# Kernel optimization log

Hardware: AMD Instinct MI355X
Metric: run time of the kernel (lower is better)

Reference implementation:

```python
import jax, jax.numpy as jnp
import numpy as np

N_SRC = [700000, 51200, 5120]
N_DST = [51200, 5120, 1024]
N_EDGE = [768000, 51200, 5120]
IN_FEATS, N_HIDDEN, N_CLASSES = 128, 256, 47


def setup_inputs() -> dict:
    key = jax.random.key(0)
    ks = jax.random.split(key, 16)
    inp = {}
    inp["x"] = jax.random.normal(ks[0], (N_SRC[0], IN_FEATS), dtype=jnp.float32)
    # edge lists per block: src indexes block-src nodes, dst indexes block-dst nodes
    for l in range(3):
        inp[f"src{l}"] = jax.random.randint(ks[1 + 2 * l], (N_EDGE[l],), 0, N_SRC[l], dtype=jnp.int32)
        inp[f"dst{l}"] = jax.random.randint(ks[2 + 2 * l], (N_EDGE[l],), 0, N_DST[l], dtype=jnp.int32)
    dims = [(IN_FEATS, N_HIDDEN), (N_HIDDEN, N_HIDDEN), (N_HIDDEN, N_CLASSES)]
    for l, (di, do) in enumerate(dims):
        scale = 1.0 / np.sqrt(di)
        inp[f"Ws{l}"] = jax.random.normal(ks[7 + 3 * l], (di, do), dtype=jnp.float32) * scale
        inp[f"Wn{l}"] = jax.random.normal(ks[8 + 3 * l], (di, do), dtype=jnp.float32) * scale
        inp[f"b{l}"] = jnp.zeros((do,), dtype=jnp.float32)
    return inp


def _sage_conv(h, src, dst, n_dst, Ws, Wn, b):
    # mean-aggregate neighbor (src) features onto dst nodes, then dual linear
    h_dst = h[:n_dst]                                   # dst nodes are a prefix of src nodes
    msg = jax.ops.segment_sum(h[src], dst, num_segments=n_dst)
    deg = jax.ops.segment_sum(jnp.ones((src.shape[0], 1), h.dtype), dst, num_segments=n_dst)
    h_neigh = msg / jnp.maximum(deg, 1.0)               # zero-degree dst -> 0 (DGL convention)
    return h_dst @ Ws + h_neigh @ Wn + b


def reference(x, src0, dst0, src1, dst1, src2, dst2,
              Ws0, Wn0, b0, Ws1, Wn1, b1, Ws2, Wn2, b2):
    h = _sage_conv(x, src0, dst0, N_DST[0], Ws0, Wn0, b0)
    h = jax.nn.relu(h)  # dropout = identity in eval
    h = _sage_conv(h, src1, dst1, N_DST[1], Ws1, Wn1, b1)
    h = jax.nn.relu(h)
    h = _sage_conv(h, src2, dst2, N_DST[2], Ws2, Wn2, b2)
    return h
```

## Files before the change

kernel.cpp:

```cpp
#include <hip/hip_runtime.h>


typedef __bf16 bf16x8 __attribute__((ext_vector_type(8)));
typedef float f32x4 __attribute__((ext_vector_type(4)));

static __device__ __forceinline__ unsigned short f32_to_bf16(float f) {
    unsigned u = __float_as_uint(f);
    u += 0x7fffu + ((u >> 16) & 1u);
    return (unsigned short)(u >> 16);
}
static __device__ __forceinline__ float bf16lo(unsigned u) { return __uint_as_float(u << 16); }
static __device__ __forceinline__ float bf16hi(unsigned u) { return __uint_as_float(u & 0xffff0000u); }

__global__ void sage_prep(const float* __restrict__ Ws0, const float* __restrict__ Wn0,
                          const float* __restrict__ Ws1, const float* __restrict__ Wn1,
                          const float* __restrict__ Ws2, const float* __restrict__ Wn2,
                          unsigned short* __restrict__ WT0, unsigned short* __restrict__ WT1,
                          unsigned short* __restrict__ WT2,
                          const int* __restrict__ d0, int* __restrict__ c0,
                          const int* __restrict__ d1, int* __restrict__ c1,
                          const int* __restrict__ d2, int* __restrict__ c2) {
    const int b = blockIdx.x;
    if (b < 256) {
        int idx = b * 256 + threadIdx.x;
        int n = idx >> 8, k = idx & 255;
        float v = (k < 128) ? Ws0[(size_t)k * 256 + n] : Wn0[(size_t)(k - 128) * 256 + n];
        WT0[idx] = f32_to_bf16(v);
    } else if (b < 768) {
        int idx = (b - 256) * 256 + threadIdx.x;
        int n = idx >> 9, k = idx & 511;
        float v = (k < 256) ? Ws1[(size_t)k * 256 + n] : Wn1[(size_t)(k - 256) * 256 + n];
        WT1[idx] = f32_to_bf16(v);
    } else if (b < 862) {
        int idx = (b - 768) * 256 + threadIdx.x;
        int n = idx >> 9, k = idx & 511;
        float v = (k < 256) ? Ws2[(size_t)k * 47 + n] : Wn2[(size_t)(k - 256) * 47 + n];
        WT2[idx] = f32_to_bf16(v);
    } else if (b < 2362) {
        int i = (b - 862) * 256 + threadIdx.x;
        int2 d = ((const int2*)d0)[i];
        atomicAdd(&c0[d.x], 1);
        atomicAdd(&c0[d.y], 1);
    } else if (b < 2462) {
        int i = (b - 2362) * 256 + threadIdx.x;
        int2 d = ((const int2*)d1)[i];
        atomicAdd(&c1[d.x], 1);
        atomicAdd(&c1[d.y], 1);
    } else {
        int i = (b - 2462) * 256 + threadIdx.x;
        int2 d = ((const int2*)d2)[i];
        atomicAdd(&c2[d.x], 1);
        atomicAdd(&c2[d.y], 1);
    }
}

__launch_bounds__(1024)
__global__ void sage_scanfill(const int* __restrict__ c0, int* __restrict__ o0, int* __restrict__ u0,
                              const int* __restrict__ c1, int* __restrict__ o1, int* __restrict__ u1,
                              const int* __restrict__ c2, int* __restrict__ o2, int* __restrict__ u2,
                              int* __restrict__ sync,
                              const int* __restrict__ s0, const int* __restrict__ d0, int* __restrict__ r0,
                              const int* __restrict__ s1, const int* __restrict__ d1, int* __restrict__ r1,
                              const int* __restrict__ s2, const int* __restrict__ d2, int* __restrict__ r2) {
    const int b = blockIdx.x;
    const int tid = threadIdx.x;
    const int lane = tid & 63;
    const int wid = tid >> 6;
    const int* counts; int* off; int* cur; int chunk, first, nblk, n;
    if (b < 50)      { counts = c0; off = o0; cur = u0; chunk = b;      first = 0;  nblk = 50; n = 51200; }
    else if (b < 55) { counts = c1; off = o1; cur = u1; chunk = b - 50; first = 50; nblk = 5;  n = 5120;  }
    else             { counts = c2; off = o2; cur = u2; chunk = 0;      first = 55; nblk = 1;  n = 1024;  }

    const int idx = chunk * 1024 + tid;
    const int v = counts[idx];

    int incl = v;
#pragma unroll
    for (int d = 1; d < 64; d <<= 1) {
        int t = __shfl_up(incl, d, 64);
        if (lane >= d) incl += t;
    }

    __shared__ int wsum[16];
    __shared__ int s_base;
    if (lane == 63) wsum[wid] = incl;
    __syncthreads();

    if (tid < 64) {
        int s = (lane < 16) ? wsum[lane] : 0;
        int inc = s;
#pragma unroll
        for (int d = 1; d < 16; d <<= 1) {
            int t = __shfl_up(inc, d, 64);
            if (lane >= d) inc += t;
        }
        if (lane < 16) wsum[lane] = inc - s;
        if (lane == 15) {
            __hip_atomic_store(&sync[16 + b], inc, __ATOMIC_RELEASE, __HIP_MEMORY_SCOPE_AGENT);
            __hip_atomic_fetch_add(&sync[0], 1, __ATOMIC_RELEASE, __HIP_MEMORY_SCOPE_AGENT);
        }
    }
    if (tid == 0) {
        while (__hip_atomic_load(&sync[0], __ATOMIC_ACQUIRE, __HIP_MEMORY_SCOPE_AGENT) < 56)
            __builtin_amdgcn_s_sleep(2);
    }
    __syncthreads();

    if (tid < 64) {
        int p = (lane < chunk)
            ? __hip_atomic_load(&sync[16 + first + lane], __ATOMIC_RELAXED, __HIP_MEMORY_SCOPE_AGENT)
            : 0;
#pragma unroll
        for (int d = 32; d >= 1; d >>= 1) p += __shfl_down(p, d, 64);
        if (lane == 0) s_base = p;
    }
    __syncthreads();

    const int excl = s_base + wsum[wid] + (incl - v);
    off[idx] = excl;
    __hip_atomic_store(&cur[idx], excl, __ATOMIC_RELAXED, __HIP_MEMORY_SCOPE_AGENT);
    if (chunk == nblk - 1 && tid == 1023) off[n] = excl + v;

    __syncthreads();
    if (tid == 0) {
        __hip_atomic_fetch_add(&sync[1], 1, __ATOMIC_RELEASE, __HIP_MEMORY_SCOPE_AGENT);
        while (__hip_atomic_load(&sync[1], __ATOMIC_ACQUIRE, __HIP_MEMORY_SCOPE_AGENT) < 56)
            __builtin_amdgcn_s_sleep(2);
    }
    __syncthreads();

    const int gtid = b * 1024 + tid;
    for (int i = gtid; i < 412160; i += 57344) {
        const int* sp; const int* dp; int* up; int* rp; int ii;
        if (i < 384000)      { sp = s0; dp = d0; up = u0; rp = r0; ii = i; }
        else if (i < 409600) { sp = s1; dp = d1; up = u1; rp = r1; ii = i - 384000; }
        else                 { sp = s2; dp = d2; up = u2; rp = r2; ii = i - 409600; }
        int2 s = ((const int2*)sp)[ii];
        int2 d = ((const int2*)dp)[ii];
        int p0 = atomicAdd(&up[d.x], 1);
        int p1 = atomicAdd(&up[d.y], 1);
        rp[p0] = s.x;
        rp[p1] = s.y;
    }
}

__global__ void sage_gather0(const float* __restrict__ x, const int* __restrict__ csr,
                             const int* __restrict__ off, unsigned short* __restrict__ out,
                             int n_dst) {
    int row = (blockIdx.x * 256 + threadIdx.x) >> 6;
    if (row >= n_dst) return;
    const int lane = threadIdx.x & 63;
    const int half = lane >> 5;
    const int fl = lane & 31;
    const int beg = off[row], end = off[row + 1];
    const float4* hp = (const float4*)x + fl;
    float4 accA = make_float4(0.f, 0.f, 0.f, 0.f);
    float4 accB = make_float4(0.f, 0.f, 0.f, 0.f);
    int i = beg;
    for (; i + 7 < end; i += 8) {
        int s0 = csr[i + half];
        int s1 = csr[i + 2 + half];
        int s2 = csr[i + 4 + half];
        int s3 = csr[i + 6 + half];
        float4 v0 = hp[(size_t)s0 * 32];
        float4 v1 = hp[(size_t)s1 * 32];
        float4 v2 = hp[(size_t)s2 * 32];
        float4 v3 = hp[(size_t)s3 * 32];
        accA.x += v0.x; accA.y += v0.y; accA.z += v0.z; accA.w += v0.w;
        accB.x += v1.x; accB.y += v1.y; accB.z += v1.z; accB.w += v1.w;
        accA.x += v2.x; accA.y += v2.y; accA.z += v2.z; accA.w += v2.w;
        accB.x += v3.x; accB.y += v3.y; accB.z += v3.z; accB.w += v3.w;
    }
    for (; i + 1 < end; i += 2) {
        int s = csr[i + half];
        float4 v = hp[(size_t)s * 32];
        accA.x += v.x; accA.y += v.y; accA.z += v.z; accA.w += v.w;
    }
    if (i < end && half == 0) {
        int s = csr[i];
        float4 v = hp[(size_t)s * 32];
        accA.x += v.x; accA.y += v.y; accA.z += v.z; accA.w += v.w;
    }
    accA.x += accB.x; accA.y += accB.y; accA.z += accB.z; accA.w += accB.w;
    accA.x += __shfl_down(accA.x, 32);
    accA.y += __shfl_down(accA.y, 32);
    accA.z += __shfl_down(accA.z, 32);
    accA.w += __shfl_down(accA.w, 32);
    if (half == 0) {
        float inv = 1.0f / fmaxf((float)(end - beg), 1.0f);
        uint2 o;
        o.x = (unsigned)f32_to_bf16(accA.x * inv) | ((unsigned)f32_to_bf16(accA.y * inv) << 16);
        o.y = (unsigned)f32_to_bf16(accA.z * inv) | ((unsigned)f32_to_bf16(accA.w * inv) << 16);
        ((uint2*)out)[(size_t)row * 32 + fl] = o;
    }
}

__global__ void sage_gather256(const unsigned short* __restrict__ h, const int* __restrict__ csr,
                               const int* __restrict__ off, unsigned short* __restrict__ out,
                               int n_dst) {
    int row = (blockIdx.x * 256 + threadIdx.x) >> 6;
    if (row >= n_dst) return;
    const int lane = threadIdx.x & 63;
    const int half = lane >> 5;
    const int fl = lane & 31;
    const int beg = off[row], end = off[row + 1];
    const uint4* hp = (const uint4*)h + fl;
    float a[8] = {0.f, 0.f, 0.f, 0.f, 0.f, 0.f, 0.f, 0.f};
    float b[8] = {0.f, 0.f, 0.f, 0.f, 0.f, 0.f, 0.f, 0.f};
    int i = beg;
    for (; i + 3 < end; i += 4) {
        int s0 = csr[i + half];
        int s1 = csr[i + 2 + half];
        uint4 u0 = hp[(size_t)s0 * 32];
        uint4 u1 = hp[(size_t)s1 * 32];
        a[0] += bf16lo(u0.x); a[1] += bf16hi(u0.x);
        a[2] += bf16lo(u0.y); a[3] += bf16hi(u0.y);
        a[4] += bf16lo(u0.z); a[5] += bf16hi(u0.z);
        a[6] += bf16lo(u0.w); a[7] += bf16hi(u0.w);
        b[0] += bf16lo(u1.x); b[1] += bf16hi(u1.x);
        b[2] += bf16lo(u1.y); b[3] += bf16hi(u1.y);
        b[4] += bf16lo(u1.z); b[5] += bf16hi(u1.z);
        b[6] += bf16lo(u1.w); b[7] += bf16hi(u1.w);
    }
    for (; i + 1 < end; i += 2) {
        int s = csr[i + half];
        uint4 u = hp[(size_t)s * 32];
        a[0] += bf16lo(u.x); a[1] += bf16hi(u.x);
        a[2] += bf16lo(u.y); a[3] += bf16hi(u.y);
        a[4] += bf16lo(u.z); a[5] += bf16hi(u.z);
        a[6] += bf16lo(u.w); a[7] += bf16hi(u.w);
    }
    if (i < end && half == 0) {
        int s = csr[i];
        uint4 u = hp[(size_t)s * 32];
        a[0] += bf16lo(u.x); a[1] += bf16hi(u.x);
        a[2] += bf16lo(u.y); a[3] += bf16hi(u.y);
        a[4] += bf16lo(u.z); a[5] += bf16hi(u.z);
        a[6] += bf16lo(u.w); a[7] += bf16hi(u.w);
    }
#pragma unroll
    for (int k = 0; k < 8; ++k) { a[k] += b[k]; a[k] += __shfl_down(a[k], 32); }
    if (half == 0) {
        float inv = 1.0f / fmaxf((float)(end - beg), 1.0f);
        uint4 o;
        o.x = (unsigned)f32_to_bf16(a[0] * inv) | ((unsigned)f32_to_bf16(a[1] * inv) << 16);
        o.y = (unsigned)f32_to_bf16(a[2] * inv) | ((unsigned)f32_to_bf16(a[3] * inv) << 16);
        o.z = (unsigned)f32_to_bf16(a[4] * inv) | ((unsigned)f32_to_bf16(a[5] * inv) << 16);
        o.w = (unsigned)f32_to_bf16(a[6] * inv) | ((unsigned)f32_to_bf16(a[7] * inv) << 16);
        ((uint4*)out)[(size_t)row * 32 + fl] = o;
    }
}

template <int RELU, int OUT_BF16, int A_FP32>
__launch_bounds__(256)
__global__ void sage_gemm(const unsigned short* __restrict__ Hdst,
                          const float* __restrict__ Hdst32,
                          const unsigned short* __restrict__ Hneigh,
                          const unsigned short* __restrict__ WT,
                          const float* __restrict__ bias,
                          void* __restrict__ Out,
                          int N, int K1) {
    const int Ktot = 2 * K1;
    __shared__ unsigned short smem[2][128][72];
    unsigned short (*As)[72] = smem[0];
    unsigned short (*Bs)[72] = smem[1];

    const int t = threadIdx.x;
    const int lane = t & 63;
    const int w = t >> 6;
    const int wm = (w >> 1) * 64;
    const int wn = (w & 1) * 64;
    const int bm = blockIdx.y * 128;
    const int bn = blockIdx.x * 128;

    const int rowL = t >> 1;
    const int kL = (t & 1) * 32;

    f32x4 acc[4][4] = {};

    const int ktiles = Ktot >> 6;
    for (int kt = 0; kt < ktiles; ++kt) {
        const int k0 = kt << 6;
        if (A_FP32 && k0 < K1) {
            const float* src = Hdst32 + (size_t)(bm + rowL) * K1 + k0 + kL;
#pragma unroll
            for (int q = 0; q < 4; ++q) {
                float4 fa = ((const float4*)src)[q * 2];
                float4 fb = ((const float4*)src)[q * 2 + 1];
                uint4 o;
                o.x = (unsigned)f32_to_bf16(fa.x) | ((unsigned)f32_to_bf16(fa.y) << 16);
                o.y = (unsigned)f32_to_bf16(fa.z) | ((unsigned)f32_to_bf16(fa.w) << 16);
                o.z = (unsigned)f32_to_bf16(fb.x) | ((unsigned)f32_to_bf16(fb.y) << 16);
                o.w = (unsigned)f32_to_bf16(fb.z) | ((unsigned)f32_to_bf16(fb.w) << 16);
                *(uint4*)&As[rowL][kL + q * 8] = o;
            }
        } else {
            const unsigned short* src = (k0 < K1)
                ? (Hdst + (size_t)(bm + rowL) * K1 + k0 + kL)
                : (Hneigh + (size_t)(bm + rowL) * K1 + (k0 - K1) + kL);
            uint4 v0 = *(const uint4*)src;
            uint4 v1 = *(const uint4*)(src + 8);
            uint4 v2 = *(const uint4*)(src + 16);
            uint4 v3 = *(const uint4*)(src + 24);
            *(uint4*)&As[rowL][kL]      = v0;
            *(uint4*)&As[rowL][kL + 8]  = v1;
            *(uint4*)&As[rowL][kL + 16] = v2;
            *(uint4*)&As[rowL][kL + 24] = v3;
        }
        {
            int n = bn + rowL;
            uint4 v0 = {0,0,0,0}, v1 = {0,0,0,0}, v2 = {0,0,0,0}, v3 = {0,0,0,0};
            if (n < N) {
                const unsigned short* srcB = WT + (size_t)n * Ktot + k0 + kL;
                v0 = *(const uint4*)srcB;
                v1 = *(const uint4*)(srcB + 8);
                v2 = *(const uint4*)(srcB + 16);
                v3 = *(const uint4*)(srcB + 24);
            }
            *(uint4*)&Bs[rowL][kL]      = v0;
            *(uint4*)&Bs[rowL][kL + 8]  = v1;
            *(uint4*)&Bs[rowL][kL + 16] = v2;
            *(uint4*)&Bs[rowL][kL + 24] = v3;
        }
        __syncthreads();

        const int fr = lane & 15;
        const int fk = (lane >> 4) * 8;
#pragma unroll
        for (int ks = 0; ks < 64; ks += 32) {
            bf16x8 av[4], bv[4];
#pragma unroll
            for (int mt = 0; mt < 4; ++mt) av[mt] = *(const bf16x8*)&As[wm + mt * 16 + fr][ks + fk];
#pragma unroll
            for (int nt = 0; nt < 4; ++nt) bv[nt] = *(const bf16x8*)&Bs[wn + nt * 16 + fr][ks + fk];
#pragma unroll
            for (int mt = 0; mt < 4; ++mt)
#pragma unroll
                for (int nt = 0; nt < 4; ++nt)
                    acc[mt][nt] = __builtin_amdgcn_mfma_f32_16x16x32_bf16(av[mt], bv[nt], acc[mt][nt], 0, 0, 0);
        }
        __syncthreads();
    }

    const int quad = lane >> 4;
    const int colL = lane & 15;
    if (OUT_BF16 && N == 256) {
        unsigned short* C = (unsigned short*)smem;
#pragma unroll
        for (int mt = 0; mt < 4; ++mt)
#pragma unroll
            for (int nt = 0; nt < 4; ++nt)
#pragma unroll
                for (int r = 0; r < 4; ++r) {
                    int lrow = wm + mt * 16 + quad * 4 + r;
                    int lcol = wn + nt * 16 + colL;
                    float v = acc[mt][nt][r] + bias[bn + lcol];
                    if (RELU) v = fmaxf(v, 0.0f);
                    C[lrow * 136 + lcol] = f32_to_bf16(v);
                }
        __syncthreads();
        unsigned short* o = (unsigned short*)Out;
#pragma unroll
        for (int c = 0; c < 8; ++c) {
            int chunk = t * 8 + c;
            int row = chunk >> 4, cc = chunk & 15;
            uint4 v = *(const uint4*)&C[row * 136 + cc * 8];
            *(uint4*)(o + (size_t)(bm + row) * N + bn + cc * 8) = v;
        }
    } else {
#pragma unroll
        for (int mt = 0; mt < 4; ++mt)
#pragma unroll
            for (int nt = 0; nt < 4; ++nt)
#pragma unroll
                for (int r = 0; r < 4; ++r) {
                    int grow = bm + wm + mt * 16 + quad * 4 + r;
                    int gcol = bn + wn + nt * 16 + colL;
                    if (gcol < N) {
                        float v = acc[mt][nt][r] + bias[gcol];
                        if (RELU) v = fmaxf(v, 0.0f);
                        if (OUT_BF16) ((unsigned short*)Out)[(size_t)grow * N + gcol] = f32_to_bf16(v);
                        else ((float*)Out)[(size_t)grow * N + gcol] = v;
                    }
                }
    }
}


extern "C" void kernel_launch(void* const* d_in, const int* in_sizes, int n_in,
                              void* d_out, int out_size, void* d_ws, size_t ws_size,
                              hipStream_t stream) {
    const float* x    = (const float*)d_in[0];
    const int* src0 = (const int*)d_in[1];
    const int* dst0 = (const int*)d_in[2];
    const int* src1 = (const int*)d_in[3];
    const int* dst1 = (const int*)d_in[4];
    const int* src2 = (const int*)d_in[5];
    const int* dst2 = (const int*)d_in[6];
    const float* Ws0 = (const float*)d_in[7];
    const float* Wn0 = (const float*)d_in[8];
    const float* b0  = (const float*)d_in[9];
    const float* Ws1 = (const float*)d_in[10];
    const float* Wn1 = (const float*)d_in[11];
    const float* b1  = (const float*)d_in[12];
    const float* Ws2 = (const float*)d_in[13];
    const float* Wn2 = (const float*)d_in[14];
    const float* b2  = (const float*)d_in[15];
    float* out = (float*)d_out;

    char* ws = (char*)d_ws;
    unsigned short* h1      = (unsigned short*)(ws + 13107200);
    unsigned short* h2      = (unsigned short*)(ws + 39321600);
    unsigned short* hneigh0 = (unsigned short*)(ws + 41943040);
    unsigned short* hneigh1 = (unsigned short*)(ws + 55050240);
    unsigned short* hneigh2 = (unsigned short*)(ws + 57671680);
    unsigned short* WT0     = (unsigned short*)(ws + 58195968);
    unsigned short* WT1     = (unsigned short*)(ws + 58327040);
    unsigned short* WT2     = (unsigned short*)(ws + 58589184);
    int* counts0 = (int*)(ws + 58637312);
    int* counts1 = (int*)(ws + 58842112);
    int* counts2 = (int*)(ws + 58862592);
    int* syncp   = (int*)(ws + 58866688);
    int* off0    = (int*)(ws + 58870784);
    int* off1    = (int*)(ws + 59075600);
    int* off2    = (int*)(ws + 59096096);
    int* cur0    = (int*)(ws + 59100208);
    int* cur1    = (int*)(ws + 59305008);
    int* cur2    = (int*)(ws + 59325488);
    int* csr0    = (int*)(ws + 59329584);
    int* csr1    = (int*)(ws + 62401584);
    int* csr2    = (int*)(ws + 62606384);

    hipMemsetAsync(counts0, 0, 233472, stream);

    sage_prep<<<2472, 256, 0, stream>>>(Ws0, Wn0, Ws1, Wn1, Ws2, Wn2,
                                        WT0, WT1, WT2,
                                        dst0, counts0, dst1, counts1, dst2, counts2);
    sage_scanfill<<<56, 1024, 0, stream>>>(counts0, off0, cur0, counts1, off1, cur1,
                                           counts2, off2, cur2, syncp,
                                           src0, dst0, csr0,
                                           src1, dst1, csr1,
                                           src2, dst2, csr2);

    sage_gather0<<<12800, 256, 0, stream>>>(x, csr0, off0, hneigh0, 51200);
    { dim3 g(2, 400); sage_gemm<1, 1, 1><<<g, 256, 0, stream>>>(nullptr, x, hneigh0, WT0, b0, h1, 256, 128); }

    sage_gather256<<<1280, 256, 0, stream>>>(h1, csr1, off1, hneigh1, 5120);
    { dim3 g(2, 40); sage_gemm<1, 1, 0><<<g, 256, 0, stream>>>(h1, nullptr, hneigh1, WT1, b1, h2, 256, 256); }

    sage_gather256<<<256, 256, 0, stream>>>(h2, csr2, off2, hneigh2, 1024);
    { dim3 g(1, 8); sage_gemm<0, 0, 0><<<g, 256, 0, stream>>>(h2, nullptr, hneigh2, WT2, b2, out, 47, 256); }
}
```

Measured before the change: 669.0 us.

## Fuse weight prep, degree count, scan and CSR fill into one grid-synced kernel

Merges the separate prep and scan/fill kernels into one persistent 256×1024 kernel that uses global atomic barriers between phases. The CSR fill now runs across all 256 blocks instead of 56. The same kernel also pre-casts the first 51200 rows of x to bf16, so the layer-0 GEMM reads bf16 instead of converting fp32 inline. This removes a launch and widens the atomic-bound fill phase. In exchange it adds an extra pass over x, more grid-wide spin barriers, and relies on all 256 large blocks being resident at once.

```diff
diff --git a/kernel.cpp b/kernel.cpp
--- a/kernel.cpp
+++ b/kernel.cpp
@@ -12,125 +12,143 @@
 static __device__ __forceinline__ float bf16lo(unsigned u) { return __uint_as_float(u << 16); }
 static __device__ __forceinline__ float bf16hi(unsigned u) { return __uint_as_float(u & 0xffff0000u); }
 
-__global__ void sage_prep(const float* __restrict__ Ws0, const float* __restrict__ Wn0,
-                          const float* __restrict__ Ws1, const float* __restrict__ Wn1,
-                          const float* __restrict__ Ws2, const float* __restrict__ Wn2,
-                          unsigned short* __restrict__ WT0, unsigned short* __restrict__ WT1,
-                          unsigned short* __restrict__ WT2,
-                          const int* __restrict__ d0, int* __restrict__ c0,
-                          const int* __restrict__ d1, int* __restrict__ c1,
-                          const int* __restrict__ d2, int* __restrict__ c2) {
-    const int b = blockIdx.x;
-    if (b < 256) {
-        int idx = b * 256 + threadIdx.x;
-        int n = idx >> 8, k = idx & 255;
-        float v = (k < 128) ? Ws0[(size_t)k * 256 + n] : Wn0[(size_t)(k - 128) * 256 + n];
-        WT0[idx] = f32_to_bf16(v);
-    } else if (b < 768) {
-        int idx = (b - 256) * 256 + threadIdx.x;
-        int n = idx >> 9, k = idx & 511;
-        float v = (k < 256) ? Ws1[(size_t)k * 256 + n] : Wn1[(size_t)(k - 256) * 256 + n];
-        WT1[idx] = f32_to_bf16(v);
-    } else if (b < 862) {
-        int idx = (b - 768) * 256 + threadIdx.x;
-        int n = idx >> 9, k = idx & 511;
-        float v = (k < 256) ? Ws2[(size_t)k * 47 + n] : Wn2[(size_t)(k - 256) * 47 + n];
-        WT2[idx] = f32_to_bf16(v);
-    } else if (b < 2362) {
-        int i = (b - 862) * 256 + threadIdx.x;
-        int2 d = ((const int2*)d0)[i];
-        atomicAdd(&c0[d.x], 1);
-        atomicAdd(&c0[d.y], 1);
-    } else if (b < 2462) {
-        int i = (b - 2362) * 256 + threadIdx.x;
-        int2 d = ((const int2*)d1)[i];
-        atomicAdd(&c1[d.x], 1);
-        atomicAdd(&c1[d.y], 1);
-    } else {
-        int i = (b - 2462) * 256 + threadIdx.x;
-        int2 d = ((const int2*)d2)[i];
-        atomicAdd(&c2[d.x], 1);
-        atomicAdd(&c2[d.y], 1);
-    }
-}
-
 __launch_bounds__(1024)
-__global__ void sage_scanfill(const int* __restrict__ c0, int* __restrict__ o0, int* __restrict__ u0,
-                              const int* __restrict__ c1, int* __restrict__ o1, int* __restrict__ u1,
-                              const int* __restrict__ c2, int* __restrict__ o2, int* __restrict__ u2,
-                              int* __restrict__ sync,
-                              const int* __restrict__ s0, const int* __restrict__ d0, int* __restrict__ r0,
-                              const int* __restrict__ s1, const int* __restrict__ d1, int* __restrict__ r1,
-                              const int* __restrict__ s2, const int* __restrict__ d2, int* __restrict__ r2) {
+__global__ void sage_csr(const float* __restrict__ x, unsigned short* __restrict__ xcast,
+                         const float* __restrict__ Ws0, const float* __restrict__ Wn0,
+                         const float* __restrict__ Ws1, const float* __restrict__ Wn1,
+                         const float* __restrict__ Ws2, const float* __restrict__ Wn2,
+                         unsigned short* __restrict__ WT0, unsigned short* __restrict__ WT1,
+                         unsigned short* __restrict__ WT2,
+                         const int* __restrict__ s0, const int* __restrict__ d0,
+                         const int* __restrict__ s1, const int* __restrict__ d1,
+                         const int* __restrict__ s2, const int* __restrict__ d2,
+                         int* __restrict__ c0, int* __restrict__ o0, int* __restrict__ u0,
+                         int* __restrict__ c1, int* __restrict__ o1, int* __restrict__ u1,
+                         int* __restrict__ c2, int* __restrict__ o2, int* __restrict__ u2,
+                         int* __restrict__ r0, int* __restrict__ r1, int* __restrict__ r2,
+                         int* __restrict__ sync) {
     const int b = blockIdx.x;
     const int tid = threadIdx.x;
-    const int lane = tid & 63;
-    const int wid = tid >> 6;
-    const int* counts; int* off; int* cur; int chunk, first, nblk, n;
-    if (b < 50)      { counts = c0; off = o0; cur = u0; chunk = b;      first = 0;  nblk = 50; n = 51200; }
-    else if (b < 55) { counts = c1; off = o1; cur = u1; chunk = b - 50; first = 50; nblk = 5;  n = 5120;  }
-    else             { counts = c2; off = o2; cur = u2; chunk = 0;      first = 55; nblk = 1;  n = 1024;  }
-
-    const int idx = chunk * 1024 + tid;
-    const int v = counts[idx];
-
-    int incl = v;
-#pragma unroll
-    for (int d = 1; d < 64; d <<= 1) {
-        int t = __shfl_up(incl, d, 64);
-        if (lane >= d) incl += t;
-    }
-
-    __shared__ int wsum[16];
-    __shared__ int s_base;
-    if (lane == 63) wsum[wid] = incl;
-    __syncthreads();
-
-    if (tid < 64) {
-        int s = (lane < 16) ? wsum[lane] : 0;
-        int inc = s;
-#pragma unroll
-        for (int d = 1; d < 16; d <<= 1) {
-            int t = __shfl_up(inc, d, 64);
-            if (lane >= d) inc += t;
-        }
-        if (lane < 16) wsum[lane] = inc - s;
-        if (lane == 15) {
-            __hip_atomic_store(&sync[16 + b], inc, __ATOMIC_RELEASE, __HIP_MEMORY_SCOPE_AGENT);
-            __hip_atomic_fetch_add(&sync[0], 1, __ATOMIC_RELEASE, __HIP_MEMORY_SCOPE_AGENT);
-        }
-    }
-    if (tid == 0) {
-        while (__hip_atomic_load(&sync[0], __ATOMIC_ACQUIRE, __HIP_MEMORY_SCOPE_AGENT) < 56)
-            __builtin_amdgcn_s_sleep(2);
-    }
-    __syncthreads();
-
-    if (tid < 64) {
-        int p = (lane < chunk)
-            ? __hip_atomic_load(&sync[16 + first + lane], __ATOMIC_RELAXED, __HIP_MEMORY_SCOPE_AGENT)
-            : 0;
-#pragma unroll
-        for (int d = 32; d >= 1; d >>= 1) p += __shfl_down(p, d, 64);
-        if (lane == 0) s_base = p;
-    }
-    __syncthreads();
-
-    const int excl = s_base + wsum[wid] + (incl - v);
-    off[idx] = excl;
-    __hip_atomic_store(&cur[idx], excl, __ATOMIC_RELAXED, __HIP_MEMORY_SCOPE_AGENT);
-    if (chunk == nblk - 1 && tid == 1023) off[n] = excl + v;
+    const int gtid = b * 1024 + tid;
+
+    for (int u = gtid; u < 2271232; u += 262144) {
+        if (u < 1638400) {
+            float4 v = ((const float4*)x)[u];
+            uint2 o;
+            o.x = (unsigned)f32_to_bf16(v.x) | ((unsigned)f32_to_bf16(v.y) << 16);
+            o.y = (unsigned)f32_to_bf16(v.z) | ((unsigned)f32_to_bf16(v.w) << 16);
+            ((uint2*)xcast)[u] = o;
+        } else if (u < 1859072) {
+            int i = u - 1638400;
+            if (i < 65536) {
+                int n = i >> 8, k = i & 255;
+                float v = (k < 128) ? Ws0[(size_t)k * 256 + n] : Wn0[(size_t)(k - 128) * 256 + n];
+                WT0[i] = f32_to_bf16(v);
+            } else if (i < 196608) {
+                int j = i - 65536;
+                int n = j >> 9, k = j & 511;
+                float v = (k < 256) ? Ws1[(size_t)k * 256 + n] : Wn1[(size_t)(k - 256) * 256 + n];
+                WT1[j] = f32_to_bf16(v);
+            } else {
+                int j = i - 196608;
+                int n = j >> 9, k = j & 511;
+                float v = (k < 256) ? Ws2[(size_t)k * 47 + n] : Wn2[(size_t)(k - 256) * 47 + n];
+                WT2[j] = f32_to_bf16(v);
+            }
+        } else {
+            int p = u - 1859072;
+            if (p < 384000) {
+                int2 d = ((const int2*)d0)[p];
+                atomicAdd(&c0[d.x], 1);
+                atomicAdd(&c0[d.y], 1);
+            } else if (p < 409600) {
+                int2 d = ((const int2*)d1)[p - 384000];
+                atomicAdd(&c1[d.x], 1);
+                atomicAdd(&c1[d.y], 1);
+            } else {
+                int2 d = ((const int2*)d2)[p - 409600];
+                atomicAdd(&c2[d.x], 1);
+                atomicAdd(&c2[d.y], 1);
+            }
+        }
+    }
 
     __syncthreads();
     if (tid == 0) {
-        __hip_atomic_fetch_add(&sync[1], 1, __ATOMIC_RELEASE, __HIP_MEMORY_SCOPE_AGENT);
-        while (__hip_atomic_load(&sync[1], __ATOMIC_ACQUIRE, __HIP_MEMORY_SCOPE_AGENT) < 56)
+        __hip_atomic_fetch_add(&sync[0], 1, __ATOMIC_RELEASE, __HIP_MEMORY_SCOPE_AGENT);
+        while (__hip_atomic_load(&sync[0], __ATOMIC_ACQUIRE, __HIP_MEMORY_SCOPE_AGENT) < 256)
             __builtin_amdgcn_s_sleep(2);
     }
     __syncthreads();
 
-    const int gtid = b * 1024 + tid;
-    for (int i = gtid; i < 412160; i += 57344) {
+    if (b < 56) {
+        const int lane = tid & 63;
+        const int wid = tid >> 6;
+        const int* counts; int* off; int* cur; int chunk, first, nblk, n;
+        if (b < 50)      { counts = c0; off = o0; cur = u0; chunk = b;      first = 0;  nblk = 50; n = 51200; }
+        else if (b < 55) { counts = c1; off = o1; cur = u1; chunk = b - 50; first = 50; nblk = 5;  n = 5120;  }
+        else             { counts = c2; off = o2; cur = u2; chunk = 0;      first = 55; nblk = 1;  n = 1024;  }
+
+        const int idx = chunk * 1024 + tid;
+        const int v = __hip_atomic_load(&counts[idx], __ATOMIC_RELAXED, __HIP_MEMORY_SCOPE_AGENT);
+
+        int incl = v;
+#pragma unroll
+        for (int d = 1; d < 64; d <<= 1) {
+            int t = __shfl_up(incl, d, 64);
+            if (lane >= d) incl += t;
+        }
+
+        __shared__ int wsum[16];
+        __shared__ int s_base;
+        if (lane == 63) wsum[wid] = incl;
+        __syncthreads();
+
+        if (tid < 64) {
+            int s = (lane < 16) ? wsum[lane] : 0;
+            int inc = s;
+#pragma unroll
+            for (int d = 1; d < 16; d <<= 1) {
+                int t = __shfl_up(inc, d, 64);
+                if (lane >= d) inc += t;
+            }
+            if (lane < 16) wsum[lane] = inc - s;
+            if (lane == 15) {
+                __hip_atomic_store(&sync[16 + b], inc, __ATOMIC_RELEASE, __HIP_MEMORY_SCOPE_AGENT);
+                __hip_atomic_fetch_add(&sync[1], 1, __ATOMIC_RELEASE, __HIP_MEMORY_SCOPE_AGENT);
+            }
+        }
+        if (tid == 0) {
+            while (__hip_atomic_load(&sync[1], __ATOMIC_ACQUIRE, __HIP_MEMORY_SCOPE_AGENT) < 56)
+                __builtin_amdgcn_s_sleep(2);
+        }
+        __syncthreads();
+
+        if (tid < 64) {
+            int p = (lane < chunk)
+                ? __hip_atomic_load(&sync[16 + first + lane], __ATOMIC_RELAXED, __HIP_MEMORY_SCOPE_AGENT)
+                : 0;
+#pragma unroll
+            for (int d = 32; d >= 1; d >>= 1) p += __shfl_down(p, d, 64);
+            if (lane == 0) s_base = p;
+        }
+        __syncthreads();
+
+        const int excl = s_base + wsum[wid] + (incl - v);
+        off[idx] = excl;
+        __hip_atomic_store(&cur[idx], excl, __ATOMIC_RELAXED, __HIP_MEMORY_SCOPE_AGENT);
+        if (chunk == nblk - 1 && tid == 1023) off[n] = excl + v;
+        __syncthreads();
+    }
+
+    if (tid == 0) {
+        __hip_atomic_fetch_add(&sync[2], 1, __ATOMIC_RELEASE, __HIP_MEMORY_SCOPE_AGENT);
+        while (__hip_atomic_load(&sync[2], __ATOMIC_ACQUIRE, __HIP_MEMORY_SCOPE_AGENT) < 256)
+            __builtin_amdgcn_s_sleep(2);
+    }
+    __syncthreads();
+
+    for (int i = gtid; i < 412160; i += 262144) {
         const int* sp; const int* dp; int* up; int* rp; int ii;
         if (i < 384000)      { sp = s0; dp = d0; up = u0; rp = r0; ii = i; }
         else if (i < 409600) { sp = s1; dp = d1; up = u1; rp = r1; ii = i - 384000; }
@@ -251,10 +269,9 @@
     }
 }
 
-template <int RELU, int OUT_BF16, int A_FP32>
+template <int RELU, int OUT_BF16>
 __launch_bounds__(256)
 __global__ void sage_gemm(const unsigned short* __restrict__ Hdst,
-                          const float* __restrict__ Hdst32,
                           const unsigned short* __restrict__ Hneigh,
                           const unsigned short* __restrict__ WT,
                           const float* __restrict__ bias,
@@ -281,20 +298,7 @@
     const int ktiles = Ktot >> 6;
     for (int kt = 0; kt < ktiles; ++kt) {
         const int k0 = kt << 6;
-        if (A_FP32 && k0 < K1) {
-            const float* src = Hdst32 + (size_t)(bm + rowL) * K1 + k0 + kL;
-#pragma unroll
-            for (int q = 0; q < 4; ++q) {
-                float4 fa = ((const float4*)src)[q * 2];
-                float4 fb = ((const float4*)src)[q * 2 + 1];
-                uint4 o;
-                o.x = (unsigned)f32_to_bf16(fa.x) | ((unsigned)f32_to_bf16(fa.y) << 16);
-                o.y = (unsigned)f32_to_bf16(fa.z) | ((unsigned)f32_to_bf16(fa.w) << 16);
-                o.z = (unsigned)f32_to_bf16(fb.x) | ((unsigned)f32_to_bf16(fb.y) << 16);
-                o.w = (unsigned)f32_to_bf16(fb.z) | ((unsigned)f32_to_bf16(fb.w) << 16);
-                *(uint4*)&As[rowL][kL + q * 8] = o;
-            }
-        } else {
+        {
             const unsigned short* src = (k0 < K1)
                 ? (Hdst + (size_t)(bm + rowL) * K1 + k0 + kL)
                 : (Hneigh + (size_t)(bm + rowL) * K1 + (k0 - K1) + kL);
@@ -409,6 +413,7 @@
     float* out = (float*)d_out;
 
     char* ws = (char*)d_ws;
+    unsigned short* xcast   = (unsigned short*)(ws + 0);
     unsigned short* h1      = (unsigned short*)(ws + 13107200);
     unsigned short* h2      = (unsigned short*)(ws + 39321600);
     unsigned short* hneigh0 = (unsigned short*)(ws + 41943040);
@@ -433,21 +438,20 @@
 
     hipMemsetAsync(counts0, 0, 233472, stream);
 
-    sage_prep<<<2472, 256, 0, stream>>>(Ws0, Wn0, Ws1, Wn1, Ws2, Wn2,
-                                        WT0, WT1, WT2,
-                                        dst0, counts0, dst1, counts1, dst2, counts2);
-    sage_scanfill<<<56, 1024, 0, stream>>>(counts0, off0, cur0, counts1, off1, cur1,
-                                           counts2, off2, cur2, syncp,
-                                           src0, dst0, csr0,
-                                           src1, dst1, csr1,
-                                           src2, dst2, csr2);
+    sage_csr<<<256, 1024, 0, stream>>>(x, xcast, Ws0, Wn0, Ws1, Wn1, Ws2, Wn2,
+                                       WT0, WT1, WT2,
+                                       src0, dst0, src1, dst1, src2, dst2,
+                                       counts0, off0, cur0,
+                                       counts1, off1, cur1,
+                                       counts2, off2, cur2,
+                                       csr0, csr1, csr2, syncp);
 
     sage_gather0<<<12800, 256, 0, stream>>>(x, csr0, off0, hneigh0, 51200);
-    { dim3 g(2, 400); sage_gemm<1, 1, 1><<<g, 256, 0, stream>>>(nullptr, x, hneigh0, WT0, b0, h1, 256, 128); }
+    { dim3 g(2, 400); sage_gemm<1, 1><<<g, 256, 0, stream>>>(xcast, hneigh0, WT0, b0, h1, 256, 128); }
 
     sage_gather256<<<1280, 256, 0, stream>>>(h1, csr1, off1, hneigh1, 5120);
-    { dim3 g(2, 40); sage_gemm<1, 1, 0><<<g, 256, 0, stream>>>(h1, nullptr, hneigh1, WT1, b1, h2, 256, 256); }
+    { dim3 g(2, 40); sage_gemm<1, 1><<<g, 256, 0, stream>>>(h1, hneigh1, WT1, b1, h2, 256, 256); }
 
     sage_gather256<<<256, 256, 0, stream>>>(h2, csr2, off2, hneigh2, 1024);
-    { dim3 g(1, 8); sage_gemm<0, 0, 0><<<g, 256, 0, stream>>>(h2, nullptr, hneigh2, WT2, b2, out, 47, 256); }
-}
+    { dim3 g(1, 8); sage_gemm<0, 0><<<g, 256, 0, stream>>>(h2, hneigh2, WT2, b2, out, 47, 256); }
+}
```

Result: slower. 696.7 us (+4.1%).
